# Performance work log

Hardware: AMD Instinct MI355X
Metric: run time of the kernel (lower is better)

The kernel has to match this reference:

```python
import jax, jax.numpy as jnp
import numpy as np
from functools import partial

D, H, W = 32, 256, 256   # grid_size (D, H, W)
V = 40000                # number of active voxels
C_IN, C_OUT = 16, 32
K = 3                    # kernel size
P = 32                   # max_points per voxel
EPS = 1e-5               # BatchNorm eps


def setup_inputs() -> dict:
    key = jax.random.key(0)
    k1, k2, k3, k4 = jax.random.split(key, 4)
    voxels = jax.random.normal(k1, (V, C_IN, P), dtype=jnp.float32)
    lin = jax.random.choice(k2, D * H * W, (V,), replace=False)
    d = (lin // (H * W)).astype(jnp.int32)
    h = ((lin // W) % H).astype(jnp.int32)
    w = (lin % W).astype(jnp.int32)
    indices = jnp.stack([w, h, d], axis=1)  # columns are (w, h, d) per original usage
    conv_w = jax.random.normal(k3, (C_OUT, C_IN, K, K, K), dtype=jnp.float32) * 0.05
    conv_b = jax.random.normal(k4, (C_OUT,), dtype=jnp.float32) * 0.05
    gamma = jnp.ones((C_OUT,), dtype=jnp.float32)
    beta = jnp.zeros((C_OUT,), dtype=jnp.float32)
    return {"voxels": voxels, "indices": indices, "conv_w": conv_w,
            "conv_b": conv_b, "gamma": gamma, "beta": beta, "batch_size": 1}


def reference(voxels, indices, conv_w, conv_b, gamma, beta, batch_size):
    # voxel features: mean over points  [V, C]
    feats = voxels.mean(axis=2)
    w_i, h_i, d_i = indices[:, 0], indices[:, 1], indices[:, 2]
    # original: batch_mask = indices[:,0] >= 0, plus per-dim bounds check
    valid = ((w_i >= 0) & (w_i < W) & (h_i >= 0) & (h_i < H) & (d_i >= 0) & (d_i < D))
    d_s = jnp.where(valid, d_i, D)  # route invalid rows out-of-bounds -> dropped
    # fused scatter replacing the python per-voxel loop; [D, H, W, C]
    grid = jnp.zeros((D, H, W, C_IN), dtype=voxels.dtype).at[d_s, h_i, w_i].set(
        feats, mode="drop")
    # same scatter is written into every batch slice in the original
    dense = jnp.broadcast_to(jnp.transpose(grid, (3, 0, 1, 2))[None],
                             (batch_size, C_IN, D, H, W))
    # Conv3d, padding = K//2 (SAME)
    out = jax.lax.conv_general_dilated(
        dense, conv_w, window_strides=(1, 1, 1), padding=[(K // 2, K // 2)] * 3,
        dimension_numbers=("NCDHW", "OIDHW", "NCDHW"))
    out = out + conv_b[None, :, None, None, None]
    # BatchNorm3d (training-mode batch statistics, biased variance)
    mean = out.mean(axis=(0, 2, 3, 4), keepdims=True)
    var = out.var(axis=(0, 2, 3, 4), keepdims=True)
    out = (out - mean) * jax.lax.rsqrt(var + EPS)
    out = out * gamma[None, :, None, None, None] + beta[None, :, None, None, None]
    return jax.nn.relu(out)
```

## Files before the change

### kernel.cpp

```cpp
#include <hip/hip_runtime.h>

#define D_   32
#define H_   256
#define W_   256
#define HW_  (H_ * W_)
#define DHW_ (D_ * H_ * W_)
#define V_   40000
#define CIN  16
#define COUT 32
#define P_   32
#define EPS_ 1e-5f

#define TD 2
#define TH 8
#define TW 32
#define NTX (W_ / TW)
#define NTY (H_ / TH)
#define NTZ (D_ / TD)
#define NT  (NTX * NTY * NTZ)
#define TPOS (TD * TH * TW)
#define OH 8
#define NQ (COUT / OH)
#define TROW 9
#define TCT 512
#define SSLOT 64
#define TAPC 640
#define VBLK ((V_ + 255) / 256)
#define WTN  (NQ * 27 * 4 * OH)
#define WTBLK ((WTN + 255) / 256)
#define FPBLK ((V_ * 4 + 255) / 256)

__global__ void prep_kernel(const int* __restrict__ idxs, int* __restrict__ tapcnt,
                            const float* __restrict__ conv_w, float4* __restrict__ wt4,
                            const float* __restrict__ vox, float4* __restrict__ feats4) {
    int b = blockIdx.x;
    int t = threadIdx.x;
    if (b < VBLK) {
        int v = b * 256 + t;
        if (v >= V_) return;
        int w = idxs[3 * v], h = idxs[3 * v + 1], d = idxs[3 * v + 2];
        if (!((unsigned)w < W_ && (unsigned)h < H_ && (unsigned)d < D_)) return;
        int dlo = max(d - 1, 0), dhi = min(d + 1, D_ - 1);
        int hlo = max(h - 1, 0), hhi = min(h + 1, H_ - 1);
        int wlo = max(w - 1, 0), whi = min(w + 1, W_ - 1);
        for (int tz = dlo / TD; tz <= dhi / TD; ++tz) {
            int zl = max(dlo, tz * TD), zh = min(dhi, tz * TD + TD - 1);
            for (int ty = hlo / TH; ty <= hhi / TH; ++ty) {
                int yl = max(hlo, ty * TH), yh = min(hhi, ty * TH + TH - 1);
                for (int tx = wlo / TW; tx <= whi / TW; ++tx) {
                    int xl = max(wlo, tx * TW), xh = min(whi, tx * TW + TW - 1);
                    int cnt = (zh - zl + 1) * (yh - yl + 1) * (xh - xl + 1);
                    atomicAdd(&tapcnt[tz * NTY * NTX + ty * NTX + tx], cnt);
                }
            }
        }
        return;
    }
    b -= VBLK;
    if (b < WTBLK) {
        int n = b * 256 + t;
        if (n < WTN) {
            int oo = n & 7;
            int jj = (n >> 3) & 3;
            int m  = n >> 5;
            int k  = m % 27;
            int quarter = m / 27;
            int o = quarter * OH + oo;
            float4 wv;
            wv.x = conv_w[(o * CIN + 4 * jj + 0) * 27 + k];
            wv.y = conv_w[(o * CIN + 4 * jj + 1) * 27 + k];
            wv.z = conv_w[(o * CIN + 4 * jj + 2) * 27 + k];
            wv.w = conv_w[(o * CIN + 4 * jj + 3) * 27 + k];
            wt4[n] = wv;
        }
        return;
    }
    b -= WTBLK;
    int idx = b * 256 + t;
    int v = idx >> 2, q = idx & 3;
    const float* base = vox + ((size_t)v * CIN + 4 * q) * P_;
    float m[4];
#pragma unroll
    for (int c = 0; c < 4; ++c) {
        const float4* p = (const float4*)(base + c * P_);
        float s = 0.f;
#pragma unroll
        for (int j = 0; j < P_ / 4; ++j) {
            float4 tv = p[j];
            s += tv.x + tv.y + tv.z + tv.w;
        }
        m[c] = s * (1.0f / (float)P_);
    }
    feats4[v * 4 + q] = make_float4(m[0], m[1], m[2], m[3]);
}

__global__ void scan_kernel(const int* __restrict__ counts, int* __restrict__ starts,
                            int* __restrict__ cursor, float* __restrict__ stats) {
    __shared__ int part[256];
    int t = threadIdx.x;
    for (int j = t; j < 2 * COUT * SSLOT; j += 256) stats[j] = 0.f;
    int base = t * 16;
    int s = 0;
    for (int j = 0; j < 16; ++j) s += counts[base + j];
    part[t] = s;
    __syncthreads();
    for (int off = 1; off < 256; off <<= 1) {
        int val = part[t];
        int add = (t >= off) ? part[t - off] : 0;
        __syncthreads();
        part[t] = val + add;
        __syncthreads();
    }
    int run = (t > 0) ? part[t - 1] : 0;
    for (int j = 0; j < 16; ++j) {
        starts[base + j] = run;
        cursor[base + j] = run;
        run += counts[base + j];
    }
}

__global__ void tap_fill_kernel(const int* __restrict__ idxs, int* __restrict__ cursor,
                                int* __restrict__ tapbuf) {
    int v = blockIdx.x * 256 + threadIdx.x;
    if (v >= V_) return;
    int w = idxs[3 * v], h = idxs[3 * v + 1], d = idxs[3 * v + 2];
    if (!((unsigned)w < W_ && (unsigned)h < H_ && (unsigned)d < D_)) return;
    int dlo = max(d - 1, 0), dhi = min(d + 1, D_ - 1);
    int hlo = max(h - 1, 0), hhi = min(h + 1, H_ - 1);
    int wlo = max(w - 1, 0), whi = min(w + 1, W_ - 1);
    for (int tz = dlo / TD; tz <= dhi / TD; ++tz) {
        int zl = max(dlo, tz * TD), zh = min(dhi, tz * TD + TD - 1);
        for (int ty = hlo / TH; ty <= hhi / TH; ++ty) {
            int yl = max(hlo, ty * TH), yh = min(hhi, ty * TH + TH - 1);
            for (int tx = wlo / TW; tx <= whi / TW; ++tx) {
                int xl = max(wlo, tx * TW), xh = min(whi, tx * TW + TW - 1);
                int cnt = (zh - zl + 1) * (yh - yl + 1) * (xh - xl + 1);
                int p = atomicAdd(&cursor[tz * NTY * NTX + ty * NTX + tx], cnt);
                for (int dq = zl; dq <= zh; ++dq)
                    for (int hq = yl; hq <= yh; ++hq)
                        for (int wq = xl; wq <= xh; ++wq) {
                            int k = ((d - dq + 1) * 3 + (h - hq + 1)) * 3 + (w - wq + 1);
                            int pos = ((dq & (TD - 1)) * TH + (hq & (TH - 1))) * TW
                                    + (wq & (TW - 1));
                            tapbuf[p++] = (v << 14) | (k << 9) | pos;
                        }
            }
        }
    }
}

__global__ void __launch_bounds__(TCT, 8) tile_conv_kernel(
    const float4* __restrict__ feats4, const float4* __restrict__ wt4,
    const int* __restrict__ tapstart, const int* __restrict__ tapcnt,
    const int* __restrict__ tapbuf, float* __restrict__ stats,
    float* __restrict__ out)
{
    __shared__ float  tile[TPOS * TROW];
    __shared__ float4 wsm4[27 * 4 * OH];
    __shared__ int    taps_l[TAPC];
    __shared__ int    taps_s[TAPC];
    __shared__ int    khist[32];
    __shared__ float  wsum[8][OH], wsq[8][OH];

    int t = threadIdx.x;
    int tile_id = blockIdx.x;
    int gs = tapstart[tile_id];
    int nt = tapcnt[tile_id];
    int tx = tile_id % NTX, ty = (tile_id / NTX) % NTY, tz = tile_id / (NTX * NTY);
    int w0 = tx * TW, h0 = ty * TH, d0 = tz * TD;
    int sl = tile_id & (SSLOT - 1);

    int ntl = min(nt, TAPC);
    if (t < 32) khist[t] = 0;
    for (int j = t; j < ntl; j += TCT) taps_l[j] = tapbuf[gs + j];
    __syncthreads();
    for (int j = t; j < ntl; j += TCT)
        atomicAdd(&khist[(taps_l[j] >> 9) & 31], 1);
    __syncthreads();
    if (t < 64) {
        int x = (t < 27) ? khist[t] : 0;
        int orig = x;
#pragma unroll
        for (int off = 1; off < 32; off <<= 1) {
            int y = __shfl_up(x, off);
            if (t >= off) x += y;
        }
        if (t < 27) khist[t] = x - orig;
    }
    __syncthreads();
    for (int j = t; j < ntl; j += TCT) {
        int tap = taps_l[j];
        int p = atomicAdd(&khist[(tap >> 9) & 31], 1);
        taps_s[p] = tap;
    }
    __syncthreads();

    int oo = t & 7, slot = t >> 3;
    int wave = t >> 6, lane = t & 63;
    int wl = t & 31, rem = t >> 5;
    size_t outb = (size_t)(d0 + (rem >> 3)) * HW_ + (size_t)(h0 + (rem & 7)) * W_
                + (size_t)(w0 + wl);
    int posD = (rem * TW + wl) * TROW;

#pragma unroll
    for (int qq = 0; qq < NQ; ++qq) {
        int obase = qq * OH;
        for (int j = t; j < TPOS * TROW / 4; j += TCT)
            ((float4*)tile)[j] = make_float4(0, 0, 0, 0);
        for (int j = t; j < 27 * 4 * OH; j += TCT)
            wsm4[j] = wt4[qq * (27 * 4 * OH) + j];
        __syncthreads();

        for (int j = slot; j < nt; j += 64) {
            unsigned tap = (unsigned)((j < TAPC) ? taps_s[j] : tapbuf[gs + j]);
            int pos = tap & 511;
            int k = (tap >> 9) & 31;
            int src = tap >> 14;
            const float4* fp = feats4 + (size_t)src * 4;
            float4 f0 = fp[0], f1 = fp[1], f2 = fp[2], f3 = fp[3];
            const float4* wp = &wsm4[k * 32 + oo];
            float4 q0 = wp[0], q1 = wp[8], q2 = wp[16], q3 = wp[24];
            float acc = q0.x * f0.x + q0.y * f0.y + q0.z * f0.z + q0.w * f0.w
                      + q1.x * f1.x + q1.y * f1.y + q1.z * f1.z + q1.w * f1.w
                      + q2.x * f2.x + q2.y * f2.y + q2.z * f2.z + q2.w * f2.w
                      + q3.x * f3.x + q3.y * f3.y + q3.z * f3.z + q3.w * f3.w;
            atomicAdd(&tile[pos * TROW + oo], acc);
        }
        __syncthreads();

        float s1 = 0.f, s2 = 0.f;
        for (int p = slot; p < TPOS; p += 64) {
            float sv = tile[p * TROW + oo];
            s1 += sv;
            s2 += sv * sv;
        }
        s1 += __shfl_xor(s1, 8);  s2 += __shfl_xor(s2, 8);
        s1 += __shfl_xor(s1, 16); s2 += __shfl_xor(s2, 16);
        s1 += __shfl_xor(s1, 32); s2 += __shfl_xor(s2, 32);
        if (lane < OH) { wsum[wave][lane] = s1; wsq[wave][lane] = s2; }

#pragma unroll
        for (int i = 0; i < OH; ++i)
            out[(size_t)(obase + i) * DHW_ + outb] = tile[posD + i];
        __syncthreads();

        if (t < OH) {
            float a = 0.f, b = 0.f;
#pragma unroll
            for (int wv = 0; wv < 8; ++wv) { a += wsum[wv][t]; b += wsq[wv][t]; }
            atomicAdd(&stats[(obase + t) * SSLOT + sl], a);
            atomicAdd(&stats[COUT * SSLOT + (obase + t) * SSLOT + sl], b);
        }
    }
}

__global__ void __launch_bounds__(256) norm_kernel(float* __restrict__ out,
                                                   const float* __restrict__ stats,
                                                   const float* __restrict__ gamma,
                                                   const float* __restrict__ beta) {
    __shared__ float sAB[2];
    int t = threadIdx.x;
    int bid = blockIdx.x;
    int c = bid >> 7;
    if (t < 64) {
        float a = stats[c * SSLOT + t];
        float b = stats[COUT * SSLOT + c * SSLOT + t];
        a += __shfl_xor(a, 1);  b += __shfl_xor(b, 1);
        a += __shfl_xor(a, 2);  b += __shfl_xor(b, 2);
        a += __shfl_xor(a, 4);  b += __shfl_xor(b, 4);
        a += __shfl_xor(a, 8);  b += __shfl_xor(b, 8);
        a += __shfl_xor(a, 16); b += __shfl_xor(b, 16);
        a += __shfl_xor(a, 32); b += __shfl_xor(b, 32);
        if (t == 0) {
            float n = (float)DHW_;
            float m1 = a / n, m2 = b / n;
            float var = fmaxf(m2 - m1 * m1, 0.f);
            float inv = rsqrtf(var + EPS_);
            float A = gamma[c] * inv;
            sAB[0] = A;
            sAB[1] = -m1 * A + beta[c];
        }
    }
    __syncthreads();
    float A = sAB[0], B = sAB[1];
    const int CH4 = DHW_ / 4;
    int base4 = c * CH4 + (bid & 127) * (CH4 / 128);
    float4* o4 = (float4*)out;
#pragma unroll
    for (int i = 0; i < 16; ++i) {
        int idx4 = base4 + i * 256 + t;
        float4 x = o4[idx4];
        x.x = fmaxf(x.x * A + B, 0.f);
        x.y = fmaxf(x.y * A + B, 0.f);
        x.z = fmaxf(x.z * A + B, 0.f);
        x.w = fmaxf(x.w * A + B, 0.f);
        o4[idx4] = x;
    }
}

extern "C" void kernel_launch(void* const* d_in, const int* in_sizes, int n_in,
                              void* d_out, int out_size, void* d_ws, size_t ws_size,
                              hipStream_t stream) {
    const float* voxels  = (const float*)d_in[0];
    const int*   indices = (const int*)  d_in[1];
    const float* conv_w  = (const float*)d_in[2];
    const float* gamma   = (const float*)d_in[4];
    const float* beta    = (const float*)d_in[5];
    float* out = (float*)d_out;

    float4* wt4      = (float4*)d_ws;
    float*  stats    = (float*)(wt4 + WTN);
    float*  mi       = stats + 2 * COUT * SSLOT;
    int*    tapcnt   = (int*)(mi + 2 * COUT);
    int*    tapstart = tapcnt + NT;
    int*    tapcur   = tapstart + NT;
    float4* feats4   = (float4*)(tapcur + NT);
    int*    tapbuf   = (int*)(feats4 + (size_t)V_ * 4);
    (void)mi;

    hipMemsetAsync(tapcnt, 0, NT * sizeof(int), stream);

    prep_kernel<<<VBLK + WTBLK + FPBLK, 256, 0, stream>>>(indices, tapcnt, conv_w, wt4,
                                                          voxels, feats4);
    scan_kernel<<<1, 256, 0, stream>>>(tapcnt, tapstart, tapcur, stats);
    tap_fill_kernel<<<VBLK, 256, 0, stream>>>(indices, tapcur, tapbuf);

    tile_conv_kernel<<<NT, TCT, 0, stream>>>(feats4, wt4, tapstart, tapcnt, tapbuf,
                                             stats, out);

    norm_kernel<<<COUT * 128, 256, 0, stream>>>(out, stats, gamma, beta);
}
```

Before: 654.5 us.

## Fuse prep, scan and tap-fill kernels into one grid-barrier persistent kernel

Merges the memset, preprocessing, prefix-scan and tap-fill stages into a single kernel, with software grid-wide barriers built from an atomic counter and sleep-spin. Zeroing of tap counts and stats moves into the kernel, and only a 16-byte barrier memset remains on the host side. The aim is to remove several launch and inter-kernel drain gaps. In exchange, all 796 blocks must be co-resident or the kernel deadlocks, the spinning adds contention, and the scan stage runs on one block while the others wait.

Result: slower. 873.1 us (+33.4%).

```diff
diff --git a/kernel.cpp b/kernel.cpp
--- a/kernel.cpp
+++ b/kernel.cpp
@@ -29,36 +29,57 @@
 #define WTN  (NQ * 27 * 4 * OH)
 #define WTBLK ((WTN + 255) / 256)
 #define FPBLK ((V_ * 4 + 255) / 256)
-
-__global__ void prep_kernel(const int* __restrict__ idxs, int* __restrict__ tapcnt,
-                            const float* __restrict__ conv_w, float4* __restrict__ wt4,
-                            const float* __restrict__ vox, float4* __restrict__ feats4) {
-    int b = blockIdx.x;
-    int t = threadIdx.x;
+#define NBLK_A (VBLK + WTBLK + FPBLK)
+
+__device__ __forceinline__ void gbar(int* bar, int target) {
+    __syncthreads();
+    if (threadIdx.x == 0) {
+        __threadfence();
+        atomicAdd(bar, 1);
+        while (atomicAdd(bar, 0) < target) __builtin_amdgcn_s_sleep(15);
+        __threadfence();
+    }
+    __syncthreads();
+}
+
+__global__ void __launch_bounds__(256, 4) prep_all_kernel(
+    const int* __restrict__ idxs, int* __restrict__ tapcnt,
+    const float* __restrict__ conv_w, float4* __restrict__ wt4,
+    const float* __restrict__ vox, float4* __restrict__ feats4,
+    int* __restrict__ starts, int* __restrict__ cursor,
+    float* __restrict__ stats, int* __restrict__ tapbuf, int* __restrict__ bar)
+{
+    __shared__ int part[256];
+    int b = blockIdx.x, t = threadIdx.x;
+    int gid = b * 256 + t;
+
+    if (gid < NT) tapcnt[gid] = 0;
+    else if (gid < NT + 2 * COUT * SSLOT) stats[gid - NT] = 0.f;
+    gbar(bar, NBLK_A);
+
     if (b < VBLK) {
-        int v = b * 256 + t;
-        if (v >= V_) return;
-        int w = idxs[3 * v], h = idxs[3 * v + 1], d = idxs[3 * v + 2];
-        if (!((unsigned)w < W_ && (unsigned)h < H_ && (unsigned)d < D_)) return;
-        int dlo = max(d - 1, 0), dhi = min(d + 1, D_ - 1);
-        int hlo = max(h - 1, 0), hhi = min(h + 1, H_ - 1);
-        int wlo = max(w - 1, 0), whi = min(w + 1, W_ - 1);
-        for (int tz = dlo / TD; tz <= dhi / TD; ++tz) {
-            int zl = max(dlo, tz * TD), zh = min(dhi, tz * TD + TD - 1);
-            for (int ty = hlo / TH; ty <= hhi / TH; ++ty) {
-                int yl = max(hlo, ty * TH), yh = min(hhi, ty * TH + TH - 1);
-                for (int tx = wlo / TW; tx <= whi / TW; ++tx) {
-                    int xl = max(wlo, tx * TW), xh = min(whi, tx * TW + TW - 1);
-                    int cnt = (zh - zl + 1) * (yh - yl + 1) * (xh - xl + 1);
-                    atomicAdd(&tapcnt[tz * NTY * NTX + ty * NTX + tx], cnt);
+        int v = gid;
+        if (v < V_) {
+            int w = idxs[3 * v], h = idxs[3 * v + 1], d = idxs[3 * v + 2];
+            if ((unsigned)w < W_ && (unsigned)h < H_ && (unsigned)d < D_) {
+                int dlo = max(d - 1, 0), dhi = min(d + 1, D_ - 1);
+                int hlo = max(h - 1, 0), hhi = min(h + 1, H_ - 1);
+                int wlo = max(w - 1, 0), whi = min(w + 1, W_ - 1);
+                for (int tz = dlo / TD; tz <= dhi / TD; ++tz) {
+                    int zl = max(dlo, tz * TD), zh = min(dhi, tz * TD + TD - 1);
+                    for (int ty = hlo / TH; ty <= hhi / TH; ++ty) {
+                        int yl = max(hlo, ty * TH), yh = min(hhi, ty * TH + TH - 1);
+                        for (int tx = wlo / TW; tx <= whi / TW; ++tx) {
+                            int xl = max(wlo, tx * TW), xh = min(whi, tx * TW + TW - 1);
+                            int cnt = (zh - zl + 1) * (yh - yl + 1) * (xh - xl + 1);
+                            atomicAdd(&tapcnt[tz * NTY * NTX + ty * NTX + tx], cnt);
+                        }
+                    }
                 }
             }
         }
-        return;
-    }
-    b -= VBLK;
-    if (b < WTBLK) {
-        int n = b * 256 + t;
+    } else if (b < VBLK + WTBLK) {
+        int n = (b - VBLK) * 256 + t;
         if (n < WTN) {
             int oo = n & 7;
             int jj = (n >> 3) & 3;
@@ -73,77 +94,76 @@
             wv.w = conv_w[(o * CIN + 4 * jj + 3) * 27 + k];
             wt4[n] = wv;
         }
-        return;
-    }
-    b -= WTBLK;
-    int idx = b * 256 + t;
-    int v = idx >> 2, q = idx & 3;
-    const float* base = vox + ((size_t)v * CIN + 4 * q) * P_;
-    float m[4];
-#pragma unroll
-    for (int c = 0; c < 4; ++c) {
-        const float4* p = (const float4*)(base + c * P_);
-        float s = 0.f;
-#pragma unroll
-        for (int j = 0; j < P_ / 4; ++j) {
-            float4 tv = p[j];
-            s += tv.x + tv.y + tv.z + tv.w;
-        }
-        m[c] = s * (1.0f / (float)P_);
-    }
-    feats4[v * 4 + q] = make_float4(m[0], m[1], m[2], m[3]);
-}
-
-__global__ void scan_kernel(const int* __restrict__ counts, int* __restrict__ starts,
-                            int* __restrict__ cursor, float* __restrict__ stats) {
-    __shared__ int part[256];
-    int t = threadIdx.x;
-    for (int j = t; j < 2 * COUT * SSLOT; j += 256) stats[j] = 0.f;
-    int base = t * 16;
-    int s = 0;
-    for (int j = 0; j < 16; ++j) s += counts[base + j];
-    part[t] = s;
-    __syncthreads();
-    for (int off = 1; off < 256; off <<= 1) {
-        int val = part[t];
-        int add = (t >= off) ? part[t - off] : 0;
+    } else {
+        int idx = (b - VBLK - WTBLK) * 256 + t;
+        int v = idx >> 2, q = idx & 3;
+        const float* base = vox + ((size_t)v * CIN + 4 * q) * P_;
+        float m[4];
+#pragma unroll
+        for (int c = 0; c < 4; ++c) {
+            const float4* p = (const float4*)(base + c * P_);
+            float s = 0.f;
+#pragma unroll
+            for (int j = 0; j < P_ / 4; ++j) {
+                float4 tv = p[j];
+                s += tv.x + tv.y + tv.z + tv.w;
+            }
+            m[c] = s * (1.0f / (float)P_);
+        }
+        feats4[v * 4 + q] = make_float4(m[0], m[1], m[2], m[3]);
+    }
+    gbar(bar, 2 * NBLK_A);
+
+    if (b == 0) {
+        int base = t * 16;
+        int s = 0;
+        for (int j = 0; j < 16; ++j) s += tapcnt[base + j];
+        part[t] = s;
         __syncthreads();
-        part[t] = val + add;
-        __syncthreads();
-    }
-    int run = (t > 0) ? part[t - 1] : 0;
-    for (int j = 0; j < 16; ++j) {
-        starts[base + j] = run;
-        cursor[base + j] = run;
-        run += counts[base + j];
-    }
-}
-
-__global__ void tap_fill_kernel(const int* __restrict__ idxs, int* __restrict__ cursor,
-                                int* __restrict__ tapbuf) {
-    int v = blockIdx.x * 256 + threadIdx.x;
-    if (v >= V_) return;
-    int w = idxs[3 * v], h = idxs[3 * v + 1], d = idxs[3 * v + 2];
-    if (!((unsigned)w < W_ && (unsigned)h < H_ && (unsigned)d < D_)) return;
-    int dlo = max(d - 1, 0), dhi = min(d + 1, D_ - 1);
-    int hlo = max(h - 1, 0), hhi = min(h + 1, H_ - 1);
-    int wlo = max(w - 1, 0), whi = min(w + 1, W_ - 1);
-    for (int tz = dlo / TD; tz <= dhi / TD; ++tz) {
-        int zl = max(dlo, tz * TD), zh = min(dhi, tz * TD + TD - 1);
-        for (int ty = hlo / TH; ty <= hhi / TH; ++ty) {
-            int yl = max(hlo, ty * TH), yh = min(hhi, ty * TH + TH - 1);
-            for (int tx = wlo / TW; tx <= whi / TW; ++tx) {
-                int xl = max(wlo, tx * TW), xh = min(whi, tx * TW + TW - 1);
-                int cnt = (zh - zl + 1) * (yh - yl + 1) * (xh - xl + 1);
-                int p = atomicAdd(&cursor[tz * NTY * NTX + ty * NTX + tx], cnt);
-                for (int dq = zl; dq <= zh; ++dq)
-                    for (int hq = yl; hq <= yh; ++hq)
-                        for (int wq = xl; wq <= xh; ++wq) {
-                            int k = ((d - dq + 1) * 3 + (h - hq + 1)) * 3 + (w - wq + 1);
-                            int pos = ((dq & (TD - 1)) * TH + (hq & (TH - 1))) * TW
-                                    + (wq & (TW - 1));
-                            tapbuf[p++] = (v << 14) | (k << 9) | pos;
+        for (int off = 1; off < 256; off <<= 1) {
+            int val = part[t];
+            int add = (t >= off) ? part[t - off] : 0;
+            __syncthreads();
+            part[t] = val + add;
+            __syncthreads();
+        }
+        int run = (t > 0) ? part[t - 1] : 0;
+        for (int j = 0; j < 16; ++j) {
+            starts[base + j] = run;
+            cursor[base + j] = run;
+            run += tapcnt[base + j];
+        }
+    }
+    gbar(bar, 3 * NBLK_A);
+
+    if (b < VBLK) {
+        int v = gid;
+        if (v < V_) {
+            int w = idxs[3 * v], h = idxs[3 * v + 1], d = idxs[3 * v + 2];
+            if ((unsigned)w < W_ && (unsigned)h < H_ && (unsigned)d < D_) {
+                int dlo = max(d - 1, 0), dhi = min(d + 1, D_ - 1);
+                int hlo = max(h - 1, 0), hhi = min(h + 1, H_ - 1);
+                int wlo = max(w - 1, 0), whi = min(w + 1, W_ - 1);
+                for (int tz = dlo / TD; tz <= dhi / TD; ++tz) {
+                    int zl = max(dlo, tz * TD), zh = min(dhi, tz * TD + TD - 1);
+                    for (int ty = hlo / TH; ty <= hhi / TH; ++ty) {
+                        int yl = max(hlo, ty * TH), yh = min(hhi, ty * TH + TH - 1);
+                        for (int tx = wlo / TW; tx <= whi / TW; ++tx) {
+                            int xl = max(wlo, tx * TW), xh = min(whi, tx * TW + TW - 1);
+                            int cnt = (zh - zl + 1) * (yh - yl + 1) * (xh - xl + 1);
+                            int p = atomicAdd(&cursor[tz * NTY * NTX + ty * NTX + tx], cnt);
+                            for (int dq = zl; dq <= zh; ++dq)
+                                for (int hq = yl; hq <= yh; ++hq)
+                                    for (int wq = xl; wq <= xh; ++wq) {
+                                        int k = ((d - dq + 1) * 3 + (h - hq + 1)) * 3
+                                              + (w - wq + 1);
+                                        int pos = ((dq & (TD - 1)) * TH + (hq & (TH - 1))) * TW
+                                                + (wq & (TW - 1));
+                                        tapbuf[p++] = (v << 14) | (k << 9) | pos;
+                                    }
                         }
+                    }
+                }
             }
         }
     }
@@ -310,20 +330,18 @@
 
     float4* wt4      = (float4*)d_ws;
     float*  stats    = (float*)(wt4 + WTN);
-    float*  mi       = stats + 2 * COUT * SSLOT;
-    int*    tapcnt   = (int*)(mi + 2 * COUT);
+    int*    bar      = (int*)(stats + 2 * COUT * SSLOT);
+    int*    tapcnt   = (int*)(stats + 2 * COUT * SSLOT + 2 * COUT);
     int*    tapstart = tapcnt + NT;
     int*    tapcur   = tapstart + NT;
     float4* feats4   = (float4*)(tapcur + NT);
     int*    tapbuf   = (int*)(feats4 + (size_t)V_ * 4);
-    (void)mi;
-
-    hipMemsetAsync(tapcnt, 0, NT * sizeof(int), stream);
-
-    prep_kernel<<<VBLK + WTBLK + FPBLK, 256, 0, stream>>>(indices, tapcnt, conv_w, wt4,
-                                                          voxels, feats4);
-    scan_kernel<<<1, 256, 0, stream>>>(tapcnt, tapstart, tapcur, stats);
-    tap_fill_kernel<<<VBLK, 256, 0, stream>>>(indices, tapcur, tapbuf);
+
+    hipMemsetAsync(bar, 0, 16, stream);
+
+    prep_all_kernel<<<NBLK_A, 256, 0, stream>>>(indices, tapcnt, conv_w, wt4,
+                                                voxels, feats4, tapstart, tapcur,
+                                                stats, tapbuf, bar);
 
     tile_conv_kernel<<<NT, TCT, 0, stream>>>(feats4, wt4, tapstart, tapcnt, tapbuf,
                                              stats, out);
```
